# Optimization experiments

Measured on AMD Instinct MI355X. Metric: run time of the kernel, lower is better.

Reference implementation:

```python
import jax, jax.numpy as jnp
import numpy as np

D = 256      # feature_dim (d_model)
H = 4        # num_heads
N = 4096     # query nodes
M = 4096     # source nodes


def _conv1x1(W, b, x):
    # Conv1d(kernel_size=1): per-position linear over channels. x: [1, Cin, N]
    return jnp.einsum('oi,bin->bon', W, x) + b[None, :, None]


def setup_inputs() -> dict:
    key = jax.random.key(0)
    ks = jax.random.split(key, 16)
    s = 0.02
    inp = {
        'x':      jax.random.normal(ks[0], (1, D, N), jnp.float32),
        'source': jax.random.normal(ks[1], (1, D, M), jnp.float32),
        'dist':   jax.random.uniform(ks[2], (1, N, M), jnp.float32),
        'mask':   jax.random.bernoulli(ks[3], 0.5, (N, M)),
        'Wq': s * jax.random.normal(ks[4], (D, D), jnp.float32),  'bq': jnp.zeros((D,), jnp.float32),
        'Wk': s * jax.random.normal(ks[5], (D, D), jnp.float32),  'bk': jnp.zeros((D,), jnp.float32),
        'Wv': s * jax.random.normal(ks[6], (D, D), jnp.float32),  'bv': jnp.zeros((D,), jnp.float32),
        'Wm': s * jax.random.normal(ks[7], (D, D), jnp.float32),  'bm': jnp.zeros((D,), jnp.float32),
        'W1': s * jax.random.normal(ks[8], (2 * D, 2 * D), jnp.float32), 'b1': jnp.zeros((2 * D,), jnp.float32),
        'W2': s * jax.random.normal(ks[9], (D, 2 * D), jnp.float32),     'b2': jnp.zeros((D,), jnp.float32),
    }
    return inp


def reference(x, source, dist, mask, Wq, bq, Wk, bk, Wv, bv, Wm, bm, W1, b1, W2, b2):
    dim = D // H  # per-head dim; torch view(1, dim, H, -1) splits channels as (dim, H)
    q = _conv1x1(Wq, bq, x).reshape(1, dim, H, N)
    k = _conv1x1(Wk, bk, source).reshape(1, dim, H, M)
    v = _conv1x1(Wv, bv, source).reshape(1, dim, H, M)

    scores = jnp.einsum('bdhn,bdhm->bhnm', q, k) / jnp.sqrt(jnp.asarray(dim, q.dtype))
    # non-standard additive mask: global detached min scales the masked-out entries
    smin = jax.lax.stop_gradient(scores.min())
    scores = scores + smin * (~mask).astype(scores.dtype)[None, None, :, :]

    prob = jax.nn.softmax(scores, axis=-1)                       # [1,H,N,M]
    attn = jnp.einsum('bhnm,bdhm->bdhn', prob, v)                # [1,dim,H,N]
    message = _conv1x1(Wm, bm, attn.reshape(1, D, N))            # merge heads

    h = jnp.concatenate([x, message], axis=1)                    # [1,2D,N]
    h = jax.nn.relu(_conv1x1(W1, b1, h))
    y = _conv1x1(W2, b2, h)                                      # [1,D,N]
    weights = scores.mean(axis=1)                                # [1,N,M]
    return y, weights
```

## Files before the change

kernel.cpp:

```cpp
#include <hip/hip_runtime.h>
#include <hip/hip_bf16.h>
#include <math.h>

#define Dm 256
#define Hh 4
#define Nn 4096
#define Mq 4096

typedef __attribute__((ext_vector_type(8))) short bf16x8;
typedef __attribute__((ext_vector_type(4))) float f32x4;
typedef _Float16 __attribute__((ext_vector_type(4))) f16x4;

#define MFMA_BF16(a,b,c) __builtin_amdgcn_mfma_f32_16x16x32_bf16(a,b,c,0,0,0)
#define MFMA_F16x16(a,b,c) __builtin_amdgcn_mfma_f32_16x16x16f16(a,b,c,0,0,0)

#define MB (1u<<20)
#define OFF_FLAG  0
#define OFF_SMIN  64
#define OFF_PART  128
#define OFF_KMAX  2048
#define OFF_MT    4096
#define OFF_DENP  (128u<<10)
#define OFF_WB    (3u*MB/2)
#define OFF_BITS  (3u*MB)
#define OFF_QB    (5u*MB)
#define OFF_KB    (7u*MB)
#define OFF_VB    (9u*MB)
#define OFF_HCAT  (11u*MB)
#define OFF_ATTNT (15u*MB)
#define OFF_XT    (17u*MB)
#define OFF_ST    (19u*MB)
#define OFF_OPART (17u*MB)
#define OFF_H1T   (17u*MB)

#define WOFF_Q  0
#define WOFF_K  65536
#define WOFF_V  131072
#define WOFF_M  196608
#define WOFF_1  262144
#define WOFF_2  524288

__device__ __forceinline__ unsigned short f2bf(float x) {
    unsigned u = __float_as_uint(x);
    u += 0x7FFF + ((u >> 16) & 1);
    return (unsigned short)(u >> 16);
}
__device__ __forceinline__ float bf2f(unsigned short b) {
    return __uint_as_float(((unsigned)b) << 16);
}

__global__ void k_detect(const unsigned char* __restrict__ mb, int* __restrict__ flag) {
    __shared__ int c[5];
    if (threadIdx.x < 5) c[threadIdx.x] = 0;
    __syncthreads();
    for (int i = threadIdx.x; i < 16384; i += blockDim.x) {
        unsigned char b = mb[i];
        if (b) {
            atomicAdd(&c[i & 3], 1);
            if ((i & 7) == 4) atomicAdd(&c[4], 1);
        }
    }
    __syncthreads();
    if (threadIdx.x == 0) {
        int f;
        if (c[3] > 0 && c[0] == 0)          f = 3;
        else if (c[1] | c[2] | c[3])        f = 1;
        else if (c[4] > 0)                  f = 0;
        else                                f = 2;
        *flag = f;
    }
}

__global__ void k_maskbits(const void* __restrict__ mp, const int* __restrict__ flagp,
                           unsigned char* __restrict__ bits) {
    size_t i = (size_t)blockIdx.x * 256 + threadIdx.x;
    const int flag = *flagp;
    size_t base = i * 8;
    unsigned b = 0;
    if (flag == 1) {
        unsigned long long u = *(const unsigned long long*)((const unsigned char*)mp + base);
        #pragma unroll
        for (int j = 0; j < 8; j++) b |= (unsigned)(((u >> (8*j)) & 0xFFull) != 0ull) << j;
    } else if (flag == 0) {
        const int* p = (const int*)mp;
        #pragma unroll
        for (int j = 0; j < 8; j++) b |= (unsigned)(p[base + j] != 0) << j;
    } else if (flag == 3) {
        const float* p = (const float*)mp;
        #pragma unroll
        for (int j = 0; j < 8; j++) b |= (unsigned)(p[base + j] != 0.0f) << j;
    } else {
        const unsigned long long* p = (const unsigned long long*)mp;
        #pragma unroll
        for (int j = 0; j < 8; j++) b |= (unsigned)(p[base + j] != 0ull) << j;
    }
    bits[i] = (unsigned char)b;
}

__global__ __launch_bounds__(256) void k_prep(const float* __restrict__ src,
                                              unsigned short* __restrict__ dst,
                                              unsigned short* __restrict__ dst2) {
    const int l = threadIdx.x & 63, g = threadIdx.x >> 6;
    const int c = blockIdx.y * 64 + l;
    const int n0 = blockIdx.x * 32 + g * 8;
    float4 v0 = *(const float4*)(src + (size_t)c * Nn + n0);
    float4 v1 = *(const float4*)(src + (size_t)c * Nn + n0 + 4);
    float vv[8] = {v0.x, v0.y, v0.z, v0.w, v1.x, v1.y, v1.z, v1.w};
    #pragma unroll
    for (int j = 0; j < 8; j++) {
        unsigned short b = f2bf(vv[j]);
        dst[(size_t)(n0 + j) * 256 + c] = b;
        if (dst2) dst2[(size_t)(n0 + j) * 512 + c] = b;
    }
}

__global__ void k_wcast(const float* __restrict__ Wq, const float* __restrict__ Wk,
                        const float* __restrict__ Wv, const float* __restrict__ Wm,
                        const float* __restrict__ W1, const float* __restrict__ W2,
                        unsigned short* __restrict__ wb) {
    size_t i = (size_t)blockIdx.x * 256 + threadIdx.x;
    const float* s; size_t off;
    if      (i < 65536)               { s = Wq; off = i; }
    else if (i < 131072)              { s = Wk; off = i - 65536; }
    else if (i < 196608)              { s = Wv; off = i - 131072; }
    else if (i < 262144)              { s = Wm; off = i - 196608; }
    else if (i < 524288)              { s = W1; off = i - 262144; }
    else                              { s = W2; off = i - 524288; }
    wb[i] = f2bf(s[off]);
}

template<int KK>
__device__ __forceinline__ void gemm_body(const unsigned short* __restrict__ wb,
                                          const float* __restrict__ bias,
                                          const unsigned short* __restrict__ xt,
                                          void* __restrict__ out, int mode,
                                          int bx, int by) {
    const int tid = threadIdx.x, w = tid >> 6, lane = tid & 63;
    const int lg = lane >> 4, lr = lane & 15;
    const int o_base = by * 64 + w * 16;
    const int n_base = bx * 64;
    f32x4 acc[4];
    #pragma unroll
    for (int j = 0; j < 4; j++) acc[j] = (f32x4){0.f, 0.f, 0.f, 0.f};
    const unsigned short* wrow = wb + (size_t)(o_base + lr) * KK + lg * 8;
    const unsigned short* xrow = xt + (size_t)(n_base + lr) * KK + lg * 8;
    #pragma unroll
    for (int k0 = 0; k0 < KK; k0 += 32) {
        bf16x8 af = *(const bf16x8*)(wrow + k0);
        #pragma unroll
        for (int j = 0; j < 4; j++) {
            bf16x8 bfr = *(const bf16x8*)(xrow + (size_t)j * 16 * KK + k0);
            acc[j] = MFMA_BF16(af, bfr, acc[j]);
        }
    }
    float bv[4];
    #pragma unroll
    for (int r = 0; r < 4; r++) bv[r] = bias[o_base + lg * 4 + r];
    #pragma unroll
    for (int j = 0; j < 4; j++) {
        #pragma unroll
        for (int r = 0; r < 4; r++) {
            int o = o_base + lg * 4 + r;
            int n = n_base + j * 16 + lr;
            float v = acc[j][r] + bv[r];
            if (mode == 0) {
                ((float*)out)[(size_t)o * Nn + n] = v;
            } else if (mode == 1) {
                ((unsigned short*)out)[(((size_t)(o & 3)) * Nn + n) * 64 + (o >> 2)] = f2bf(v);
            } else if (mode == 2) {
                union { _Float16 h; unsigned short u; } cv; cv.h = (_Float16)v;
                ((unsigned short*)out)[(((size_t)(o & 3)) * 64 + (o >> 2)) * Mq + n] = cv.u;
            } else if (mode == 3) {
                ((unsigned short*)out)[(size_t)n * 512 + 256 + o] = f2bf(v);
            } else if (mode == 4) {
                ((unsigned short*)out)[(size_t)n * 512 + o] = f2bf(fmaxf(v, 0.f));
            } else {
                int dd = o >> 2, hh = o & 3, g = dd >> 3, pos = dd & 7;
                int slot = g ^ (n & 7);
                ((unsigned short*)out)[(((size_t)hh * Mq + n)) * 64 + slot * 8 + pos] = f2bf(v);
            }
        }
    }
}

template<int KK>
__global__ __launch_bounds__(256) void k_mgemm(const unsigned short* __restrict__ wb,
                                               const float* __restrict__ bias,
                                               const unsigned short* __restrict__ xt,
                                               void* __restrict__ out, int mode) {
    gemm_body<KK>(wb, bias, xt, out, mode, blockIdx.x, blockIdx.y);
}

__global__ __launch_bounds__(256) void k_qkv(const unsigned short* __restrict__ wb,
                                             const float* __restrict__ bq,
                                             const float* __restrict__ bk,
                                             const float* __restrict__ bv,
                                             const unsigned short* __restrict__ xt,
                                             const unsigned short* __restrict__ st,
                                             void* __restrict__ qb, void* __restrict__ kb,
                                             void* __restrict__ vb) {
    const int z = blockIdx.z;
    const float* bias = (z == 0) ? bq : ((z == 1) ? bk : bv);
    const unsigned short* X = (z == 0) ? xt : st;
    void* out = (z == 0) ? qb : ((z == 1) ? kb : vb);
    int mode = (z == 0) ? 1 : ((z == 1) ? 5 : 2);
    gemm_body<256>(wb + z * 65536, bias, X, out, mode, blockIdx.x, blockIdx.y);
}

__global__ void k_init(unsigned* __restrict__ kmax) {
    if (threadIdx.x < 4) kmax[threadIdx.x] = 0u;
}

__global__ __launch_bounds__(256) void k_knorm(const unsigned short* __restrict__ kb,
                                               unsigned* __restrict__ kmax) {
    const int h = blockIdx.y;
    const int m = blockIdx.x * 256 + threadIdx.x;
    const unsigned short* row = kb + ((size_t)(h * Mq + m) << 6);
    float s = 0.f;
    #pragma unroll
    for (int i = 0; i < 64; i++) { float v = bf2f(row[i]); s = fmaf(v, v, s); }
    __shared__ float red[256];
    red[threadIdx.x] = s;
    __syncthreads();
    for (int st = 128; st > 0; st >>= 1) {
        if (threadIdx.x < st) red[threadIdx.x] = fmaxf(red[threadIdx.x], red[threadIdx.x + st]);
        __syncthreads();
    }
    if (threadIdx.x == 0) atomicMax(kmax + h, __float_as_uint(red[0]));
}

__global__ __launch_bounds__(256) void k_qnorm(const unsigned short* __restrict__ qb,
                                               const unsigned* __restrict__ kmax,
                                               float* __restrict__ mtarr) {
    const int row = blockIdx.x * 256 + threadIdx.x;
    const unsigned short* qr = qb + ((size_t)row << 6);
    float s = 0.f;
    #pragma unroll
    for (int i = 0; i < 64; i++) { float v = bf2f(qr[i]); s = fmaf(v, v, s); }
    float k2 = __uint_as_float(kmax[row >> 12]);
    mtarr[row] = sqrtf(s * k2) * 0.125f;
}

__global__ __launch_bounds__(512) void k_min(
    const unsigned short* __restrict__ qb, const unsigned short* __restrict__ kb,
    float* __restrict__ partial) {
    __shared__ unsigned short kbuf[2][8192];
    const int tid = threadIdx.x;
    const int w = tid >> 6, lane = tid & 63;
    const int lg = lane >> 4, lr = lane & 15;
    const int n0 = blockIdx.x * 128 + w * 16;
    const int m0 = blockIdx.y * 512;

    bf16x8 qf[4][2];
    #pragma unroll
    for (int h = 0; h < 4; h++)
        #pragma unroll
        for (int kh = 0; kh < 2; kh++)
            qf[h][kh] = *(const bf16x8*)(qb + (((size_t)h * Nn + n0 + lr) << 6) + kh*32 + lg*8);

    const int h0 = tid >> 8, q0 = tid & 255;
    const unsigned short* src0 = kb + (((size_t)h0 * Mq + m0) << 6) + q0 * 8;
    const unsigned short* src1 = kb + (((size_t)(h0 + 2) * Mq + m0) << 6) + q0 * 8;
    unsigned short* dst0 = &kbuf[0][h0 * 2048 + q0 * 8];
    unsigned short* dst1 = &kbuf[0][(h0 + 2) * 2048 + q0 * 8];

    float mn = INFINITY;

    bf16x8 r0 = *(const bf16x8*)(src0);
    bf16x8 r1 = *(const bf16x8*)(src1);
    *(bf16x8*)dst0 = r0;
    *(bf16x8*)dst1 = r1;
    __syncthreads();
    r0 = *(const bf16x8*)(src0 + 2048);
    r1 = *(const bf16x8*)(src1 + 2048);

    for (int t = 0; t < 16; t++) {
        const unsigned short* kB = &kbuf[t & 1][0];
        #pragma unroll
        for (int mi = 0; mi < 2; mi++) {
            const int rowoff = (mi * 16 + lr) * 64;
            #pragma unroll
            for (int h = 0; h < 4; h++) {
                bf16x8 a0 = *(const bf16x8*)(kB + h*2048 + rowoff + ((lg ^ (lr & 7)) << 3));
                bf16x8 a1 = *(const bf16x8*)(kB + h*2048 + rowoff + (((lg + 4) ^ (lr & 7)) << 3));
                f32x4 acc = (f32x4){0.f, 0.f, 0.f, 0.f};
                acc = MFMA_BF16(a0, qf[h][0], acc);
                acc = MFMA_BF16(a1, qf[h][1], acc);
                mn = fminf(mn, fminf(fminf(acc[0], acc[1]), fminf(acc[2], acc[3])));
            }
        }
        if (t < 15) {
            *(bf16x8*)(dst0 + (((t + 1) & 1) ? 8192 : 0)) = r0;
            *(bf16x8*)(dst1 + (((t + 1) & 1) ? 8192 : 0)) = r1;
        }
        __syncthreads();
        if (t < 14) {
            r0 = *(const bf16x8*)(src0 + (size_t)(t + 2) * 2048);
            r1 = *(const bf16x8*)(src1 + (size_t)(t + 2) * 2048);
        }
    }

    for (int off = 1; off < 64; off <<= 1) mn = fminf(mn, __shfl_xor(mn, off));
    __shared__ float wmin[8];
    if (lane == 0) wmin[w] = mn;
    __syncthreads();
    if (tid == 0) {
        float m2 = wmin[0];
        #pragma unroll
        for (int i = 1; i < 8; i++) m2 = fminf(m2, wmin[i]);
        partial[blockIdx.x * 8 + blockIdx.y] = m2 * 0.125f;
    }
}

__global__ void k_minreduce(const float* __restrict__ partial, float* __restrict__ smin) {
    const int tid = threadIdx.x;
    float mn = partial[tid];
    __shared__ float red[256];
    red[tid] = mn;
    __syncthreads();
    for (int st = 128; st > 0; st >>= 1) {
        if (tid < st) red[tid] = fminf(red[tid], red[tid + st]);
        __syncthreads();
    }
    if (tid == 0) *smin = red[0];
}

__global__ __launch_bounds__(512) void k_wout(
    const unsigned short* __restrict__ qb, const unsigned short* __restrict__ kb,
    const unsigned long long* __restrict__ bits,
    const float* __restrict__ sminp, float* __restrict__ wout) {
    __shared__ unsigned short kbuf[2][8192];
    const int tid = threadIdx.x;
    const int w = tid >> 6, lane = tid & 63;
    const int lg = lane >> 4, lr = lane & 15;
    const int n0 = blockIdx.x * 128 + w * 16;
    const int m0 = blockIdx.y * 512;
    const float smin = *sminp;

    bf16x8 qf[4][2];
    #pragma unroll
    for (int h = 0; h < 4; h++)
        #pragma unroll
        for (int kh = 0; kh < 2; kh++)
            qf[h][kh] = *(const bf16x8*)(qb + (((size_t)h * Nn + n0 + lr) << 6) + kh*32 + lg*8);

    const int h0 = tid >> 8, q0 = tid & 255;
    const unsigned short* src0 = kb + (((size_t)h0 * Mq + m0) << 6) + q0 * 8;
    const unsigned short* src1 = kb + (((size_t)(h0 + 2) * Mq + m0) << 6) + q0 * 8;
    unsigned short* dst0 = &kbuf[0][h0 * 2048 + q0 * 8];
    unsigned short* dst1 = &kbuf[0][(h0 + 2) * 2048 + q0 * 8];

    const unsigned long long* brow = bits + (((size_t)(n0 + lr)) << 6) + (m0 >> 6);
    unsigned long long bw = 0ull;

    bf16x8 r0 = *(const bf16x8*)(src0);
    bf16x8 r1 = *(const bf16x8*)(src1);
    *(bf16x8*)dst0 = r0;
    *(bf16x8*)dst1 = r1;
    __syncthreads();
    r0 = *(const bf16x8*)(src0 + 2048);
    r1 = *(const bf16x8*)(src1 + 2048);

    for (int t = 0; t < 16; t++) {
        const unsigned short* kB = &kbuf[t & 1][0];
        const int mch = m0 + t * 32;
        if ((t & 1) == 0) bw = brow[t >> 1];
        #pragma unroll
        for (int mi = 0; mi < 2; mi++) {
            const int rowoff = (mi * 16 + lr) * 64;
            f32x4 accA = (f32x4){0.f, 0.f, 0.f, 0.f};
            f32x4 accB = (f32x4){0.f, 0.f, 0.f, 0.f};
            #pragma unroll
            for (int h = 0; h < 2; h++) {
                bf16x8 a0 = *(const bf16x8*)(kB + h*2048 + rowoff + ((lg ^ (lr & 7)) << 3));
                bf16x8 a1 = *(const bf16x8*)(kB + h*2048 + rowoff + (((lg + 4) ^ (lr & 7)) << 3));
                accA = MFMA_BF16(a0, qf[h][0], accA);
                accA = MFMA_BF16(a1, qf[h][1], accA);
            }
            #pragma unroll
            for (int h = 2; h < 4; h++) {
                bf16x8 a0 = *(const bf16x8*)(kB + h*2048 + rowoff + ((lg ^ (lr & 7)) << 3));
                bf16x8 a1 = *(const bf16x8*)(kB + h*2048 + rowoff + (((lg + 4) ^ (lr & 7)) << 3));
                accB = MFMA_BF16(a0, qf[h][0], accB);
                accB = MFMA_BF16(a1, qf[h][1], accB);
            }
            const int shb = (t & 1) * 32 + mi * 16 + lg * 4;
            f32x4 wv;
            #pragma unroll
            for (int r = 0; r < 4; r++) {
                bool b = (bw >> (shb + r)) & 1ull;
                wv[r] = fmaf(accA[r] + accB[r], 0.03125f, b ? 0.f : smin);
            }
            *(f32x4*)(wout + (size_t)(n0 + lr) * Mq + mch + mi * 16 + lg * 4) = wv;
        }
        if (t < 15) {
            *(bf16x8*)(dst0 + (((t + 1) & 1) ? 8192 : 0)) = r0;
            *(bf16x8*)(dst1 + (((t + 1) & 1) ? 8192 : 0)) = r1;
        }
        __syncthreads();
        if (t < 14) {
            r0 = *(const bf16x8*)(src0 + (size_t)(t + 2) * 2048);
            r1 = *(const bf16x8*)(src1 + (size_t)(t + 2) * 2048);
        }
    }
}

__global__ __launch_bounds__(512) void k_pv(
    const unsigned short* __restrict__ qb, const unsigned short* __restrict__ kb,
    const unsigned short* __restrict__ vbh,
    const unsigned long long* __restrict__ bits,
    const float* __restrict__ sminp, const float* __restrict__ mtarr,
    float* __restrict__ denp, unsigned short* __restrict__ opart) {
    __shared__ unsigned short kbuf[2][4096];
    __shared__ unsigned short vbuf[2][4096];
    const int tid = threadIdx.x;
    const int w = tid >> 6, lane = tid & 63;
    const int lg = lane >> 4, lr = lane & 15;
    const int h = blockIdx.y & 3, mb = blockIdx.y >> 2;
    const int n0 = blockIdx.x * 256 + w * 32;
    const int m0 = mb * 1024;
    const float smin = *sminp;
    const float sminc = fmaxf(smin, 0.f);

    bf16x8 qf[2][2];
    float cT[2], cF[2];
    #pragma unroll
    for (int ns = 0; ns < 2; ns++) {
        #pragma unroll
        for (int kh = 0; kh < 2; kh++)
            qf[ns][kh] = *(const bf16x8*)(qb + (((size_t)h * Nn + n0 + ns*16 + lr) << 6) + kh*32 + lg*8);
        float mtE = mtarr[(size_t)h * Nn + n0 + ns*16 + lr] + sminc;
        cT[ns] = -mtE * 1.44269504f;
        cF[ns] = cT[ns] + smin * 1.44269504f;
    }

    f32x4 oacc[2][4];
    #pragma unroll
    for (int ns = 0; ns < 2; ns++)
        #pragma unroll
        for (int ds = 0; ds < 4; ds++)
            oacc[ns][ds] = (f32x4){0.f, 0.f, 0.f, 0.f};
    float dsum[2] = {0.f, 0.f};

    const unsigned short* ksrc = kb + (((size_t)h * Mq + m0) << 6) + tid * 8;
    const int vj = tid & 7, vdd = tid >> 3;
    const unsigned short* vsrc = vbh + (size_t)(h * 64 + vdd) * Mq + m0 + vj * 8;
    const int vdst = ((vj >> 1) * 64 + vdd) * 16 + (vj & 1) * 8;

    bf16x8 rk = *(const bf16x8*)(ksrc);
    bf16x8 rv = *(const bf16x8*)(vsrc);
    *(bf16x8*)&kbuf[0][tid * 8] = rk;
    *(bf16x8*)&vbuf[0][vdst] = rv;
    __syncthreads();
    rk = *(const bf16x8*)(ksrc + 4096);
    rv = *(const bf16x8*)(vsrc + 64);

    for (int t = 0; t < 16; t++) {
        const unsigned short* kB = &kbuf[t & 1][0];
        const unsigned short* vB = &vbuf[t & 1][0];
        const int mch = m0 + t * 64;
        unsigned long long bw[2];
        #pragma unroll
        for (int ns = 0; ns < 2; ns++)
            bw[ns] = bits[(((size_t)(n0 + ns*16 + lr)) << 6) + (mch >> 6)];
        #pragma unroll
        for (int mi = 0; mi < 4; mi++) {
            const int rowoff = (mi * 16 + lr) * 64;
            bf16x8 a0 = *(const bf16x8*)(kB + rowoff + ((lg ^ (lr & 7)) << 3));
            bf16x8 a1 = *(const bf16x8*)(kB + rowoff + (((lg + 4) ^ (lr & 7)) << 3));
            f16x4 vf[4];
            #pragma unroll
            for (int ds = 0; ds < 4; ds++)
                vf[ds] = *(const f16x4*)&vB[(mi * 64 + ds * 16 + lr) * 16 + lg * 4];
            const int shb = mi * 16 + lg * 4;
            #pragma unroll
            for (int ns = 0; ns < 2; ns++) {
                f32x4 acc = (f32x4){0.f, 0.f, 0.f, 0.f};
                acc = MFMA_BF16(a0, qf[ns][0], acc);
                acc = MFMA_BF16(a1, qf[ns][1], acc);
                f16x4 pf;
                float dloc = 0.f;
                #pragma unroll
                for (int r = 0; r < 4; r++) {
                    bool b = (bw[ns] >> (shb + r)) & 1ull;
                    float p = exp2f(fmaf(acc[r], 0.18033688f, b ? cT[ns] : cF[ns]));
                    dloc += p;
                    pf[r] = (_Float16)p;
                }
                dsum[ns] += dloc;
                #pragma unroll
                for (int ds = 0; ds < 4; ds++)
                    oacc[ns][ds] = MFMA_F16x16(pf, vf[ds], oacc[ns][ds]);
            }
        }
        if (t < 15) {
            *(bf16x8*)&kbuf[(t + 1) & 1][tid * 8] = rk;
            *(bf16x8*)&vbuf[(t + 1) & 1][vdst] = rv;
        }
        __syncthreads();
        if (t < 14) {
            rk = *(const bf16x8*)(ksrc + (size_t)(t + 2) * 4096);
            rv = *(const bf16x8*)(vsrc + (size_t)(t + 2) * 64);
        }
    }

    #pragma unroll
    for (int ns = 0; ns < 2; ns++) {
        dsum[ns] += __shfl_xor(dsum[ns], 16);
        dsum[ns] += __shfl_xor(dsum[ns], 32);
    }
    if (lane < 16) {
        #pragma unroll
        for (int ns = 0; ns < 2; ns++)
            denp[((size_t)h * Nn + n0 + ns*16 + lane) * 4 + mb] = dsum[ns];
    }
    unsigned short* op = opart + (size_t)mb * (Dm * Nn);
    #pragma unroll
    for (int ns = 0; ns < 2; ns++)
        #pragma unroll
        for (int ds = 0; ds < 4; ds++) {
            int c = (ds * 16 + lr) * 4 + h;
            int n = n0 + ns * 16 + lg * 4;
            unsigned long long pk =
                (unsigned long long)f2bf(oacc[ns][ds][0]) |
                ((unsigned long long)f2bf(oacc[ns][ds][1]) << 16) |
                ((unsigned long long)f2bf(oacc[ns][ds][2]) << 32) |
                ((unsigned long long)f2bf(oacc[ns][ds][3]) << 48);
            *(unsigned long long*)&op[(size_t)c * Nn + n] = pk;
        }
}

__global__ __launch_bounds__(256) void k_finish(const unsigned short* __restrict__ opart,
                                                const float* __restrict__ denp,
                                                unsigned short* __restrict__ attnT) {
    __shared__ float t[64][65];
    const int cb = blockIdx.y * 64, nb = blockIdx.x * 64;
    const int tid = threadIdx.x;
    #pragma unroll
    for (int e = 0; e < 16; e++) {
        int idx = e * 256 + tid;
        int c_l = idx >> 6, n_l = idx & 63;
        int c = cb + c_l, n = nb + n_l;
        float s = 0.f;
        #pragma unroll
        for (int y = 0; y < 4; y++)
            s += bf2f(opart[(size_t)y * (Dm*Nn) + (size_t)c * Nn + n]);
        size_t row = (size_t)(c & 3) * Nn + n;
        float d = denp[row*4] + denp[row*4+1] + denp[row*4+2] + denp[row*4+3];
        t[c_l][n_l] = s / d;
    }
    __syncthreads();
    #pragma unroll
    for (int e = 0; e < 16; e++) {
        int idx = e * 256 + tid;
        int n_l = idx >> 6, c_l = idx & 63;
        attnT[(size_t)(nb + n_l) * 256 + cb + c_l] = f2bf(t[c_l][n_l]);
    }
}

extern "C" void kernel_launch(void* const* d_in, const int* in_sizes, int n_in,
                              void* d_out, int out_size, void* d_ws, size_t ws_size,
                              hipStream_t stream) {
    const float* x      = (const float*)d_in[0];
    const float* source = (const float*)d_in[1];
    const void*  mask   = d_in[3];
    const float* Wq = (const float*)d_in[4];  const float* bq = (const float*)d_in[5];
    const float* Wk = (const float*)d_in[6];  const float* bk = (const float*)d_in[7];
    const float* Wv = (const float*)d_in[8];  const float* bv = (const float*)d_in[9];
    const float* Wm = (const float*)d_in[10]; const float* bm = (const float*)d_in[11];
    const float* W1 = (const float*)d_in[12]; const float* b1 = (const float*)d_in[13];
    const float* W2 = (const float*)d_in[14]; const float* b2 = (const float*)d_in[15];

    float* y    = (float*)d_out;
    float* wout = y + (size_t)Dm * Nn;

    char* ws = (char*)d_ws;
    int*      flag  = (int*)(ws + OFF_FLAG);
    float*    sminp = (float*)(ws + OFF_SMIN);
    float*    part  = (float*)(ws + OFF_PART);
    unsigned* kmax  = (unsigned*)(ws + OFF_KMAX);
    float*    mtarr = (float*)(ws + OFF_MT);
    float*    denp  = (float*)(ws + OFF_DENP);
    unsigned short* wb    = (unsigned short*)(ws + OFF_WB);
    unsigned char*  bits  = (unsigned char*)(ws + OFF_BITS);
    unsigned short* qb    = (unsigned short*)(ws + OFF_QB);
    unsigned short* kb    = (unsigned short*)(ws + OFF_KB);
    unsigned short* vb    = (unsigned short*)(ws + OFF_VB);
    unsigned short* hcat  = (unsigned short*)(ws + OFF_HCAT);
    unsigned short* attnT = (unsigned short*)(ws + OFF_ATTNT);
    unsigned short* xt    = (unsigned short*)(ws + OFF_XT);
    unsigned short* st    = (unsigned short*)(ws + OFF_ST);
    unsigned short* opart = (unsigned short*)(ws + OFF_OPART);
    unsigned short* h1t   = (unsigned short*)(ws + OFF_H1T);

    k_detect<<<1, 256, 0, stream>>>((const unsigned char*)mask, flag);
    k_maskbits<<<8192, 256, 0, stream>>>(mask, flag, bits);

    k_prep<<<dim3(128, 4), 256, 0, stream>>>(x, xt, hcat);
    k_prep<<<dim3(128, 4), 256, 0, stream>>>(source, st, nullptr);
    k_wcast<<<2560, 256, 0, stream>>>(Wq, Wk, Wv, Wm, W1, W2, wb);

    k_qkv<<<dim3(64, 4, 3), 256, 0, stream>>>(wb, bq, bk, bv, xt, st, qb, kb, vb);

    k_init<<<1, 64, 0, stream>>>(kmax);
    k_knorm<<<dim3(16, 4), 256, 0, stream>>>(kb, kmax);
    k_qnorm<<<64, 256, 0, stream>>>(qb, kmax, mtarr);

    k_min<<<dim3(32, 8), 512, 0, stream>>>(qb, kb, part);
    k_minreduce<<<1, 256, 0, stream>>>(part, sminp);

    k_wout<<<dim3(32, 8), 512, 0, stream>>>(qb, kb, (const unsigned long long*)bits, sminp, wout);

    k_pv<<<dim3(16, 16), 512, 0, stream>>>(qb, kb, vb, (const unsigned long long*)bits,
                                           sminp, mtarr, denp, opart);
    k_finish<<<dim3(64, 4), 256, 0, stream>>>(opart, denp, attnT);

    k_mgemm<256><<<dim3(64, 4), 256, 0, stream>>>(wb + WOFF_M, bm, attnT, hcat, 3);
    k_mgemm<512><<<dim3(64, 8), 256, 0, stream>>>(wb + WOFF_1, b1, hcat, h1t, 4);
    k_mgemm<512><<<dim3(64, 4), 256, 0, stream>>>(wb + WOFF_2, b2, h1t, y, 0);
}
```

Measured before the change: 208.1 us.

## Double grid parallelism for min/wout/pv kernels, swizzle V LDS, merge launches

Splits k_min and k_wout into twice as many blocks along M, and halves k_pv's rows per warp so it launches twice as many blocks, in order to fill more CUs. k_pv also gets a swizzled V shared-memory layout to reduce bank conflicts, and packs its f16 conversion with cvt_pkrtz. Small launches are merged: the kmax init moves into k_detect and the two prep launches become one z-indexed launch. In exchange, K/Q fragments are reused less per block, so more redundant loads and more partial minima are produced.

```diff
diff --git a/kernel.cpp b/kernel.cpp
--- a/kernel.cpp
+++ b/kernel.cpp
@@ -10,6 +10,7 @@
 typedef __attribute__((ext_vector_type(8))) short bf16x8;
 typedef __attribute__((ext_vector_type(4))) float f32x4;
 typedef _Float16 __attribute__((ext_vector_type(4))) f16x4;
+typedef __fp16 __attribute__((ext_vector_type(2))) h16x2;
 
 #define MFMA_BF16(a,b,c) __builtin_amdgcn_mfma_f32_16x16x32_bf16(a,b,c,0,0,0)
 #define MFMA_F16x16(a,b,c) __builtin_amdgcn_mfma_f32_16x16x16f16(a,b,c,0,0,0)
@@ -17,8 +18,8 @@
 #define MB (1u<<20)
 #define OFF_FLAG  0
 #define OFF_SMIN  64
-#define OFF_PART  128
-#define OFF_KMAX  2048
+#define OFF_PART  1024
+#define OFF_KMAX  3072
 #define OFF_MT    4096
 #define OFF_DENP  (128u<<10)
 #define OFF_WB    (3u*MB/2)
@@ -49,9 +50,11 @@
     return __uint_as_float(((unsigned)b) << 16);
 }
 
-__global__ void k_detect(const unsigned char* __restrict__ mb, int* __restrict__ flag) {
+__global__ void k_detect(const unsigned char* __restrict__ mb, int* __restrict__ flag,
+                         unsigned* __restrict__ kmax) {
     __shared__ int c[5];
     if (threadIdx.x < 5) c[threadIdx.x] = 0;
+    if (threadIdx.x < 4) kmax[threadIdx.x] = 0u;
     __syncthreads();
     for (int i = threadIdx.x; i < 16384; i += blockDim.x) {
         unsigned char b = mb[i];
@@ -97,9 +100,15 @@
     bits[i] = (unsigned char)b;
 }
 
-__global__ __launch_bounds__(256) void k_prep(const float* __restrict__ src,
-                                              unsigned short* __restrict__ dst,
-                                              unsigned short* __restrict__ dst2) {
+__global__ __launch_bounds__(256) void k_prep(const float* __restrict__ x,
+                                              const float* __restrict__ source,
+                                              unsigned short* __restrict__ xt,
+                                              unsigned short* __restrict__ st,
+                                              unsigned short* __restrict__ hcat) {
+    const int z = blockIdx.z;
+    const float* src = z ? source : x;
+    unsigned short* dst = z ? st : xt;
+    unsigned short* dst2 = z ? nullptr : hcat;
     const int l = threadIdx.x & 63, g = threadIdx.x >> 6;
     const int c = blockIdx.y * 64 + l;
     const int n0 = blockIdx.x * 32 + g * 8;
@@ -207,10 +216,6 @@
     gemm_body<256>(wb + z * 65536, bias, X, out, mode, blockIdx.x, blockIdx.y);
 }
 
-__global__ void k_init(unsigned* __restrict__ kmax) {
-    if (threadIdx.x < 4) kmax[threadIdx.x] = 0u;
-}
-
 __global__ __launch_bounds__(256) void k_knorm(const unsigned short* __restrict__ kb,
                                                unsigned* __restrict__ kmax) {
     const int h = blockIdx.y;
@@ -249,7 +254,7 @@
     const int w = tid >> 6, lane = tid & 63;
     const int lg = lane >> 4, lr = lane & 15;
     const int n0 = blockIdx.x * 128 + w * 16;
-    const int m0 = blockIdx.y * 512;
+    const int m0 = blockIdx.y * 256;
 
     bf16x8 qf[4][2];
     #pragma unroll
@@ -274,7 +279,7 @@
     r0 = *(const bf16x8*)(src0 + 2048);
     r1 = *(const bf16x8*)(src1 + 2048);
 
-    for (int t = 0; t < 16; t++) {
+    for (int t = 0; t < 8; t++) {
         const unsigned short* kB = &kbuf[t & 1][0];
         #pragma unroll
         for (int mi = 0; mi < 2; mi++) {
@@ -289,12 +294,12 @@
                 mn = fminf(mn, fminf(fminf(acc[0], acc[1]), fminf(acc[2], acc[3])));
             }
         }
-        if (t < 15) {
+        if (t < 7) {
             *(bf16x8*)(dst0 + (((t + 1) & 1) ? 8192 : 0)) = r0;
             *(bf16x8*)(dst1 + (((t + 1) & 1) ? 8192 : 0)) = r1;
         }
         __syncthreads();
-        if (t < 14) {
+        if (t < 6) {
             r0 = *(const bf16x8*)(src0 + (size_t)(t + 2) * 2048);
             r1 = *(const bf16x8*)(src1 + (size_t)(t + 2) * 2048);
         }
@@ -308,13 +313,13 @@
         float m2 = wmin[0];
         #pragma unroll
         for (int i = 1; i < 8; i++) m2 = fminf(m2, wmin[i]);
-        partial[blockIdx.x * 8 + blockIdx.y] = m2 * 0.125f;
+        partial[blockIdx.x * 16 + blockIdx.y] = m2 * 0.125f;
     }
 }
 
 __global__ void k_minreduce(const float* __restrict__ partial, float* __restrict__ smin) {
     const int tid = threadIdx.x;
-    float mn = partial[tid];
+    float mn = fminf(partial[tid], partial[tid + 256]);
     __shared__ float red[256];
     red[tid] = mn;
     __syncthreads();
@@ -334,7 +339,7 @@
     const int w = tid >> 6, lane = tid & 63;
     const int lg = lane >> 4, lr = lane & 15;
     const int n0 = blockIdx.x * 128 + w * 16;
-    const int m0 = blockIdx.y * 512;
+    const int m0 = blockIdx.y * 256;
     const float smin = *sminp;
 
     bf16x8 qf[4][2];
@@ -361,7 +366,7 @@
     r0 = *(const bf16x8*)(src0 + 2048);
     r1 = *(const bf16x8*)(src1 + 2048);
 
-    for (int t = 0; t < 16; t++) {
+    for (int t = 0; t < 8; t++) {
         const unsigned short* kB = &kbuf[t & 1][0];
         const int mch = m0 + t * 32;
         if ((t & 1) == 0) bw = brow[t >> 1];
@@ -393,12 +398,12 @@
             }
             *(f32x4*)(wout + (size_t)(n0 + lr) * Mq + mch + mi * 16 + lg * 4) = wv;
         }
-        if (t < 15) {
+        if (t < 7) {
             *(bf16x8*)(dst0 + (((t + 1) & 1) ? 8192 : 0)) = r0;
             *(bf16x8*)(dst1 + (((t + 1) & 1) ? 8192 : 0)) = r1;
         }
         __syncthreads();
-        if (t < 14) {
+        if (t < 6) {
             r0 = *(const bf16x8*)(src0 + (size_t)(t + 2) * 2048);
             r1 = *(const bf16x8*)(src1 + (size_t)(t + 2) * 2048);
         }
@@ -417,117 +422,105 @@
     const int w = tid >> 6, lane = tid & 63;
     const int lg = lane >> 4, lr = lane & 15;
     const int h = blockIdx.y & 3, mb = blockIdx.y >> 2;
-    const int n0 = blockIdx.x * 256 + w * 32;
+    const int n0 = blockIdx.x * 128 + w * 16;
     const int m0 = mb * 1024;
     const float smin = *sminp;
     const float sminc = fmaxf(smin, 0.f);
 
-    bf16x8 qf[2][2];
-    float cT[2], cF[2];
-    #pragma unroll
-    for (int ns = 0; ns < 2; ns++) {
-        #pragma unroll
-        for (int kh = 0; kh < 2; kh++)
-            qf[ns][kh] = *(const bf16x8*)(qb + (((size_t)h * Nn + n0 + ns*16 + lr) << 6) + kh*32 + lg*8);
-        float mtE = mtarr[(size_t)h * Nn + n0 + ns*16 + lr] + sminc;
-        cT[ns] = -mtE * 1.44269504f;
-        cF[ns] = cT[ns] + smin * 1.44269504f;
-    }
-
-    f32x4 oacc[2][4];
-    #pragma unroll
-    for (int ns = 0; ns < 2; ns++)
-        #pragma unroll
-        for (int ds = 0; ds < 4; ds++)
-            oacc[ns][ds] = (f32x4){0.f, 0.f, 0.f, 0.f};
-    float dsum[2] = {0.f, 0.f};
+    bf16x8 qf0 = *(const bf16x8*)(qb + (((size_t)h * Nn + n0 + lr) << 6) + lg*8);
+    bf16x8 qf1 = *(const bf16x8*)(qb + (((size_t)h * Nn + n0 + lr) << 6) + 32 + lg*8);
+    float mtE = mtarr[(size_t)h * Nn + n0 + lr] + sminc;
+    const float cT = -mtE * 1.44269504f;
+    const float cF = cT + smin * 1.44269504f;
+
+    f32x4 oacc[4];
+    #pragma unroll
+    for (int ds = 0; ds < 4; ds++) oacc[ds] = (f32x4){0.f, 0.f, 0.f, 0.f};
+    float dsum = 0.f;
 
     const unsigned short* ksrc = kb + (((size_t)h * Mq + m0) << 6) + tid * 8;
-    const int vj = tid & 7, vdd = tid >> 3;
+    const int vdd = tid >> 3, vj = tid & 7;
     const unsigned short* vsrc = vbh + (size_t)(h * 64 + vdd) * Mq + m0 + vj * 8;
-    const int vdst = ((vj >> 1) * 64 + vdd) * 16 + (vj & 1) * 8;
-
+    const int vds = vdd >> 4, vlr = vdd & 15, vmi = vj >> 1;
+    const int vswz = (vlr >> 2) & 3;
+    const int vbase = ((vmi * 4 + vds) * 16 + vlr) * 4;
+    const int vdst0 = (vbase + (((vj & 1) * 2 + 0) ^ vswz)) * 4;
+    const int vdst1 = (vbase + (((vj & 1) * 2 + 1) ^ vswz)) * 4;
+
+    union { bf16x8 v; unsigned long long q[2]; } rv;
     bf16x8 rk = *(const bf16x8*)(ksrc);
-    bf16x8 rv = *(const bf16x8*)(vsrc);
+    rv.v = *(const bf16x8*)(vsrc);
     *(bf16x8*)&kbuf[0][tid * 8] = rk;
-    *(bf16x8*)&vbuf[0][vdst] = rv;
+    *(unsigned long long*)&vbuf[0][vdst0] = rv.q[0];
+    *(unsigned long long*)&vbuf[0][vdst1] = rv.q[1];
     __syncthreads();
     rk = *(const bf16x8*)(ksrc + 4096);
-    rv = *(const bf16x8*)(vsrc + 64);
+    rv.v = *(const bf16x8*)(vsrc + 64);
+
+    const unsigned long long* brow = bits + (((size_t)(n0 + lr)) << 6) + (m0 >> 6);
+    const int kslot0 = (lg ^ (lr & 7)) << 3;
+    const int kslot1 = ((lg + 4) ^ (lr & 7)) << 3;
+    const int vrslot = (lg ^ ((lr >> 2) & 3)) * 4;
 
     for (int t = 0; t < 16; t++) {
         const unsigned short* kB = &kbuf[t & 1][0];
         const unsigned short* vB = &vbuf[t & 1][0];
-        const int mch = m0 + t * 64;
-        unsigned long long bw[2];
-        #pragma unroll
-        for (int ns = 0; ns < 2; ns++)
-            bw[ns] = bits[(((size_t)(n0 + ns*16 + lr)) << 6) + (mch >> 6)];
+        unsigned long long bw = brow[t];
         #pragma unroll
         for (int mi = 0; mi < 4; mi++) {
             const int rowoff = (mi * 16 + lr) * 64;
-            bf16x8 a0 = *(const bf16x8*)(kB + rowoff + ((lg ^ (lr & 7)) << 3));
-            bf16x8 a1 = *(const bf16x8*)(kB + rowoff + (((lg + 4) ^ (lr & 7)) << 3));
+            bf16x8 a0 = *(const bf16x8*)(kB + rowoff + kslot0);
+            bf16x8 a1 = *(const bf16x8*)(kB + rowoff + kslot1);
             f16x4 vf[4];
             #pragma unroll
             for (int ds = 0; ds < 4; ds++)
-                vf[ds] = *(const f16x4*)&vB[(mi * 64 + ds * 16 + lr) * 16 + lg * 4];
+                vf[ds] = *(const f16x4*)&vB[((mi * 4 + ds) * 16 + lr) * 16 + vrslot];
+            f32x4 acc = (f32x4){0.f, 0.f, 0.f, 0.f};
+            acc = MFMA_BF16(a0, qf0, acc);
+            acc = MFMA_BF16(a1, qf1, acc);
             const int shb = mi * 16 + lg * 4;
+            float p0 = exp2f(fmaf(acc[0], 0.18033688f, ((bw >> (shb + 0)) & 1ull) ? cT : cF));
+            float p1 = exp2f(fmaf(acc[1], 0.18033688f, ((bw >> (shb + 1)) & 1ull) ? cT : cF));
+            float p2 = exp2f(fmaf(acc[2], 0.18033688f, ((bw >> (shb + 2)) & 1ull) ? cT : cF));
+            float p3 = exp2f(fmaf(acc[3], 0.18033688f, ((bw >> (shb + 3)) & 1ull) ? cT : cF));
+            dsum += (p0 + p1) + (p2 + p3);
+            union { h16x2 h2[2]; f16x4 f4; } pu;
+            pu.h2[0] = __builtin_amdgcn_cvt_pkrtz(p0, p1);
+            pu.h2[1] = __builtin_amdgcn_cvt_pkrtz(p2, p3);
+            f16x4 pf = pu.f4;
             #pragma unroll
-            for (int ns = 0; ns < 2; ns++) {
-                f32x4 acc = (f32x4){0.f, 0.f, 0.f, 0.f};
-                acc = MFMA_BF16(a0, qf[ns][0], acc);
-                acc = MFMA_BF16(a1, qf[ns][1], acc);
-                f16x4 pf;
-                float dloc = 0.f;
-                #pragma unroll
-                for (int r = 0; r < 4; r++) {
-                    bool b = (bw[ns] >> (shb + r)) & 1ull;
-                    float p = exp2f(fmaf(acc[r], 0.18033688f, b ? cT[ns] : cF[ns]));
-                    dloc += p;
-                    pf[r] = (_Float16)p;
-                }
-                dsum[ns] += dloc;
-                #pragma unroll
-                for (int ds = 0; ds < 4; ds++)
-                    oacc[ns][ds] = MFMA_F16x16(pf, vf[ds], oacc[ns][ds]);
-            }
+            for (int ds = 0; ds < 4; ds++)
+                oacc[ds] = MFMA_F16x16(pf, vf[ds], oacc[ds]);
         }
         if (t < 15) {
             *(bf16x8*)&kbuf[(t + 1) & 1][tid * 8] = rk;
-            *(bf16x8*)&vbuf[(t + 1) & 1][vdst] = rv;
+            *(unsigned long long*)&vbuf[(t + 1) & 1][vdst0] = rv.q[0];
+            *(unsigned long long*)&vbuf[(t + 1) & 1][vdst1] = rv.q[1];
         }
         __syncthreads();
         if (t < 14) {
             rk = *(const bf16x8*)(ksrc + (size_t)(t + 2) * 4096);
-            rv = *(const bf16x8*)(vsrc + (size_t)(t + 2) * 64);
-        }
-    }
-
-    #pragma unroll
-    for (int ns = 0; ns < 2; ns++) {
-        dsum[ns] += __shfl_xor(dsum[ns], 16);
-        dsum[ns] += __shfl_xor(dsum[ns], 32);
-    }
-    if (lane < 16) {
-        #pragma unroll
-        for (int ns = 0; ns < 2; ns++)
-            denp[((size_t)h * Nn + n0 + ns*16 + lane) * 4 + mb] = dsum[ns];
-    }
+            rv.v = *(const bf16x8*)(vsrc + (size_t)(t + 2) * 64);
+        }
+    }
+
+    dsum += __shfl_xor(dsum, 16);
+    dsum += __shfl_xor(dsum, 32);
+    if (lane < 16)
+        denp[((size_t)h * Nn + n0 + lane) * 4 + mb] = dsum;
+
     unsigned short* op = opart + (size_t)mb * (Dm * Nn);
     #pragma unroll
-    for (int ns = 0; ns < 2; ns++)
-        #pragma unroll
-        for (int ds = 0; ds < 4; ds++) {
-            int c = (ds * 16 + lr) * 4 + h;
-            int n = n0 + ns * 16 + lg * 4;
-            unsigned long long pk =
-                (unsigned long long)f2bf(oacc[ns][ds][0]) |
-                ((unsigned long long)f2bf(oacc[ns][ds][1]) << 16) |
-                ((unsigned long long)f2bf(oacc[ns][ds][2]) << 32) |
-                ((unsigned long long)f2bf(oacc[ns][ds][3]) << 48);
-            *(unsigned long long*)&op[(size_t)c * Nn + n] = pk;
-        }
+    for (int ds = 0; ds < 4; ds++) {
+        int c = (ds * 16 + lr) * 4 + h;
+        int n = n0 + lg * 4;
+        unsigned long long pk =
+            (unsigned long long)f2bf(oacc[ds][0]) |
+            ((unsigned long long)f2bf(oacc[ds][1]) << 16) |
+            ((unsigned long long)f2bf(oacc[ds][2]) << 32) |
+            ((unsigned long long)f2bf(oacc[ds][3]) << 48);
+        *(unsigned long long*)&op[(size_t)c * Nn + n] = pk;
+    }
 }
 
 __global__ __launch_bounds__(256) void k_finish(const unsigned short* __restrict__ opart,
@@ -593,25 +586,23 @@
     unsigned short* opart = (unsigned short*)(ws + OFF_OPART);
     unsigned short* h1t   = (unsigned short*)(ws + OFF_H1T);
 
-    k_detect<<<1, 256, 0, stream>>>((const unsigned char*)mask, flag);
+    k_detect<<<1, 256, 0, stream>>>((const unsigned char*)mask, flag, kmax);
     k_maskbits<<<8192, 256, 0, stream>>>(mask, flag, bits);
 
-    k_prep<<<dim3(128, 4), 256, 0, stream>>>(x, xt, hcat);
-    k_prep<<<dim3(128, 4), 256, 0, stream>>>(source, st, nullptr);
+    k_prep<<<dim3(128, 4, 2), 256, 0, stream>>>(x, source, xt, st, hcat);
     k_wcast<<<2560, 256, 0, stream>>>(Wq, Wk, Wv, Wm, W1, W2, wb);
 
     k_qkv<<<dim3(64, 4, 3), 256, 0, stream>>>(wb, bq, bk, bv, xt, st, qb, kb, vb);
 
-    k_init<<<1, 64, 0, stream>>>(kmax);
     k_knorm<<<dim3(16, 4), 256, 0, stream>>>(kb, kmax);
     k_qnorm<<<64, 256, 0, stream>>>(qb, kmax, mtarr);
 
-    k_min<<<dim3(32, 8), 512, 0, stream>>>(qb, kb, part);
+    k_min<<<dim3(32, 16), 512, 0, stream>>>(qb, kb, part);
     k_minreduce<<<1, 256, 0, stream>>>(part, sminp);
 
-    k_wout<<<dim3(32, 8), 512, 0, stream>>>(qb, kb, (const unsigned long long*)bits, sminp, wout);
-
-    k_pv<<<dim3(16, 16), 512, 0, stream>>>(qb, kb, vb, (const unsigned long long*)bits,
+    k_wout<<<dim3(32, 16), 512, 0, stream>>>(qb, kb, (const unsigned long long*)bits, sminp, wout);
+
+    k_pv<<<dim3(32, 16), 512, 0, stream>>>(qb, kb, vb, (const unsigned long long*)bits,
                                            sminp, mtarr, denp, opart);
     k_finish<<<dim3(64, 4), 256, 0, stream>>>(opart, denp, attnT);
 
```

Measured after the change: 198.1 us. 1.05x faster.
